# Optimization experiments

Measured on AMD Instinct MI355X. Metric: run time of the kernel, lower is better.

The kernel has to match this reference:

```python
import jax, jax.numpy as jnp
import numpy as np

T = 8            # number of tables
V = 250_000      # rows per table
D = 64           # embedding_dim
B = 16_384       # batch size
L = 20           # ids per bag (history length)


def setup_inputs() -> dict:
    key = jax.random.key(0)
    k1, k2 = jax.random.split(key)
    # local ids in [0, V) per table, then add cumulative table offset -> global ids
    local = jax.random.randint(k1, (T, B * L), 0, V)
    table_offset = (jnp.arange(T) * V)[:, None]
    indices = (local + table_offset).reshape(-1)          # [T*B*L] global ids
    offsets = jnp.arange(T * B) * L                        # bag start positions (include_last_offset=False)
    weight = jax.random.normal(k2, (T * V, D), jnp.float32) * 0.01  # all tables stacked row-wise
    return {"indices": indices, "offsets": offsets, "weight": weight}


def reference(indices, offsets, weight):
    # Equivalent math: per-table slice of indices/offsets, mean-pooled embedding
    # bag per table, concat along feature dim. Since the global weight stacks the
    # tables row-wise and indices are global, the per-table offset subtraction +
    # local gather is identical to a single global gather.
    N = indices.shape[0]
    num_bags = offsets.shape[0]            # T * B
    # bag id of each index position (offsets is sorted, bags are contiguous)
    seg = jnp.searchsorted(offsets, jnp.arange(N), side="right") - 1
    rows = weight[indices]                                      # [N, D] gather
    sums = jax.ops.segment_sum(rows, seg, num_segments=num_bags)               # [T*B, D]
    counts = jax.ops.segment_sum(jnp.ones((N,), weight.dtype), seg, num_segments=num_bags)
    pooled = sums / jnp.maximum(counts, 1.0)[:, None]           # mode='mean'
    # bags are ordered (table, batch); concat per-table outputs along dim 1
    out = jnp.moveaxis(pooled.reshape(T, num_bags // T, D), 0, 1).reshape(num_bags // T, T * D)
    return out  # [B, T*D]
```

## Files before the change

kernel.cpp:

```cpp
#include <hip/hip_runtime.h>
#include <hip/hip_bf16.h>


constexpr int D = 64;
constexpr int TD = 512;

__global__ __launch_bounds__(256)
void embag_mean_kernel(const int* __restrict__ indices,
                       const int* __restrict__ offsets,
                       const float* __restrict__ weight,
                       float* __restrict__ out,
                       int num_bags, int N, int B) {
    const int wave = (blockIdx.x * blockDim.x + threadIdx.x) >> 6;
    const int lane = threadIdx.x & 63;
    if (wave >= num_bags) return;

    const int start = offsets[wave];
    const int end   = (wave + 1 < num_bags) ? offsets[wave + 1] : N;
    const int count = end - start;

    const int sub = lane >> 4;
    const int l4  = lane & 15;

    float4 acc = make_float4(0.f, 0.f, 0.f, 0.f);

    if (count == 20) {
        const int jb = start + sub;
        const int r0 = indices[jb];
        const int r1 = indices[jb + 4];
        const int r2 = indices[jb + 8];
        const int r3 = indices[jb + 12];
        const int r4 = indices[jb + 16];
        const float4 v0 = reinterpret_cast<const float4*>(weight + (size_t)r0 * D)[l4];
        const float4 v1 = reinterpret_cast<const float4*>(weight + (size_t)r1 * D)[l4];
        const float4 v2 = reinterpret_cast<const float4*>(weight + (size_t)r2 * D)[l4];
        const float4 v3 = reinterpret_cast<const float4*>(weight + (size_t)r3 * D)[l4];
        const float4 v4 = reinterpret_cast<const float4*>(weight + (size_t)r4 * D)[l4];
        acc.x = v0.x + v1.x + v2.x + v3.x + v4.x;
        acc.y = v0.y + v1.y + v2.y + v3.y + v4.y;
        acc.z = v0.z + v1.z + v2.z + v3.z + v4.z;
        acc.w = v0.w + v1.w + v2.w + v3.w + v4.w;
    } else {
        for (int j = start + sub; j < end; j += 4) {
            const int row = indices[j];
            const float4 v = reinterpret_cast<const float4*>(weight + (size_t)row * D)[l4];
            acc.x += v.x; acc.y += v.y; acc.z += v.z; acc.w += v.w;
        }
    }

    acc.x += __shfl_xor(acc.x, 16); acc.y += __shfl_xor(acc.y, 16);
    acc.z += __shfl_xor(acc.z, 16); acc.w += __shfl_xor(acc.w, 16);
    acc.x += __shfl_xor(acc.x, 32); acc.y += __shfl_xor(acc.y, 32);
    acc.z += __shfl_xor(acc.z, 32); acc.w += __shfl_xor(acc.w, 32);

    if (sub == 0) {
        const float inv = 1.0f / fmaxf((float)count, 1.0f);
        const int t = wave / B;
        const int b = wave - t * B;
        float4 r;
        r.x = acc.x * inv; r.y = acc.y * inv; r.z = acc.z * inv; r.w = acc.w * inv;
        float4* dst = reinterpret_cast<float4*>(out + (size_t)b * TD + t * D);
        dst[l4] = r;
    }
}

extern "C" void kernel_launch(void* const* d_in, const int* in_sizes, int n_in,
                              void* d_out, int out_size, void* d_ws, size_t ws_size,
                              hipStream_t stream) {
    const int*   indices = (const int*)d_in[0];
    const int*   offsets = (const int*)d_in[1];
    const float* weight  = (const float*)d_in[2];
    float*       out     = (float*)d_out;

    const int N        = in_sizes[0];
    const int num_bags = in_sizes[1];
    const int B        = out_size / TD;

    const int waves_per_block = 256 / 64;
    const int grid = (num_bags + waves_per_block - 1) / waves_per_block;

    embag_mean_kernel<<<grid, 256, 0, stream>>>(indices, offsets, weight, out,
                                                num_bags, N, B);
}
```

Before: 647.3 us.

## Gather one float per lane with readlane-broadcast indices and nontemporal stores

Changes the per-wave mapping from four sub-groups of 16 lanes each loading float4 to all 64 lanes loading one float of each row. One coalesced load fetches all 20 indices, and readlane broadcasts each row id as a scalar. This removes the cross-lane shuffle reduction and the masked store, and writes output with nontemporal stores. The trade-off is 20 scalar-addressed 4-byte loads per lane instead of 5 vectorized float4 loads, which means more memory instructions in flight per bag.

After: 645.3 us. About the same (-0.3%).

```diff
diff --git a/kernel.cpp b/kernel.cpp
--- a/kernel.cpp
+++ b/kernel.cpp
@@ -19,49 +19,29 @@
     const int end   = (wave + 1 < num_bags) ? offsets[wave + 1] : N;
     const int count = end - start;
 
-    const int sub = lane >> 4;
-    const int l4  = lane & 15;
+    const int t = wave / B;
+    const int b = wave - t * B;
+    float* const dst = out + (size_t)b * TD + t * D + lane;
 
-    float4 acc = make_float4(0.f, 0.f, 0.f, 0.f);
+    float acc = 0.0f;
 
     if (count == 20) {
-        const int jb = start + sub;
-        const int r0 = indices[jb];
-        const int r1 = indices[jb + 4];
-        const int r2 = indices[jb + 8];
-        const int r3 = indices[jb + 12];
-        const int r4 = indices[jb + 16];
-        const float4 v0 = reinterpret_cast<const float4*>(weight + (size_t)r0 * D)[l4];
-        const float4 v1 = reinterpret_cast<const float4*>(weight + (size_t)r1 * D)[l4];
-        const float4 v2 = reinterpret_cast<const float4*>(weight + (size_t)r2 * D)[l4];
-        const float4 v3 = reinterpret_cast<const float4*>(weight + (size_t)r3 * D)[l4];
-        const float4 v4 = reinterpret_cast<const float4*>(weight + (size_t)r4 * D)[l4];
-        acc.x = v0.x + v1.x + v2.x + v3.x + v4.x;
-        acc.y = v0.y + v1.y + v2.y + v3.y + v4.y;
-        acc.z = v0.z + v1.z + v2.z + v3.z + v4.z;
-        acc.w = v0.w + v1.w + v2.w + v3.w + v4.w;
+        const int myidx = indices[start + (lane < 20 ? lane : 0)];
+        #pragma unroll
+        for (int k = 0; k < 20; ++k) {
+            const int row = __builtin_amdgcn_readlane(myidx, k);
+            acc += weight[(size_t)row * D + lane];
+        }
+        acc *= (1.0f / 20.0f);
     } else {
-        for (int j = start + sub; j < end; j += 4) {
+        for (int j = start; j < end; ++j) {
             const int row = indices[j];
-            const float4 v = reinterpret_cast<const float4*>(weight + (size_t)row * D)[l4];
-            acc.x += v.x; acc.y += v.y; acc.z += v.z; acc.w += v.w;
+            acc += weight[(size_t)row * D + lane];
         }
+        acc *= 1.0f / fmaxf((float)count, 1.0f);
     }
 
-    acc.x += __shfl_xor(acc.x, 16); acc.y += __shfl_xor(acc.y, 16);
-    acc.z += __shfl_xor(acc.z, 16); acc.w += __shfl_xor(acc.w, 16);
-    acc.x += __shfl_xor(acc.x, 32); acc.y += __shfl_xor(acc.y, 32);
-    acc.z += __shfl_xor(acc.z, 32); acc.w += __shfl_xor(acc.w, 32);
-
-    if (sub == 0) {
-        const float inv = 1.0f / fmaxf((float)count, 1.0f);
-        const int t = wave / B;
-        const int b = wave - t * B;
-        float4 r;
-        r.x = acc.x * inv; r.y = acc.y * inv; r.z = acc.z * inv; r.w = acc.w * inv;
-        float4* dst = reinterpret_cast<float4*>(out + (size_t)b * TD + t * D);
-        dst[l4] = r;
-    }
+    __builtin_nontemporal_store(acc, dst);
 }
 
 extern "C" void kernel_launch(void* const* d_in, const int* in_sizes, int n_in,
```
